# Kernel optimization log

Measured on AMD Instinct MI355X. Metric: run time of the kernel, lower is better.

Reference implementation:

```python
import jax, jax.numpy as jnp
import numpy as np

N_NODES = 50000
N_EDGES = 800000
F_DIM = 256
H_DIM = 256
O_DIM = 64


def spmm(edge_index, edge_weight, x):
    # sparse adj (COO) @ dense x: out[dst] += w * x[src]
    src = edge_index[0]
    dst = edge_index[1]
    msgs = edge_weight[:, None] * x[src]          # [E, D]
    return jax.ops.segment_sum(msgs, dst, num_segments=x.shape[0])


def setup_inputs() -> dict:
    key = jax.random.key(0)
    ks = jax.random.split(key, 10)
    stdv = 1.0 / np.sqrt(H_DIM)
    u = lambda k, shp: jax.random.uniform(k, shp, jnp.float32, -stdv, stdv)
    return {
        "input": jax.random.normal(ks[0], (N_NODES, F_DIM), jnp.float32),
        "edge_index": jax.random.randint(ks[1], (2, N_EDGES), 0, N_NODES, jnp.int32),
        "edge_weight": jax.random.uniform(ks[2], (N_EDGES,), jnp.float32),
        "mixture_weight": u(ks[3], (1,)),
        "hidden_weight": u(ks[4], (F_DIM, H_DIM)),
        "hidden_bias": u(ks[5], (H_DIM,)),
        "mean_weight": u(ks[6], (H_DIM, O_DIM)),
        "mean_bias": u(ks[7], (O_DIM,)),
        "log_std_weight": u(ks[8], (H_DIM, O_DIM)),
        "log_std_bias": u(ks[9], (O_DIM,)),
    }


def reference(input, edge_index, edge_weight, mixture_weight, hidden_weight,
              hidden_bias, mean_weight, mean_bias, log_std_weight, log_std_bias):
    # eval mode: dropout is identity
    # --- GCN branch ---
    support = input @ hidden_weight                       # [N, H]
    hidden_g = jax.nn.relu(spmm(edge_index, edge_weight, support) + hidden_bias)
    mean_gcn = spmm(edge_index, edge_weight, hidden_g @ mean_weight)      # [N, O]
    log_std_gcn = spmm(edge_index, edge_weight, hidden_g @ log_std_weight)
    # --- MLP branch ---
    hidden_m = jax.nn.relu(support + hidden_bias)
    mean_mlp = hidden_m @ mean_weight + mean_bias
    log_std_mlp = hidden_m @ log_std_weight + log_std_bias
    # --- mixture (note: z_mean uses raw weight, z_log_std uses sigmoid, as in source) ---
    mw = mixture_weight
    mr = jax.nn.sigmoid(mixture_weight)
    z_mean = mean_gcn * mw + mean_mlp * (1.0 - mw)
    z_log_std = log_std_gcn * mr + log_std_mlp * (1.0 - mr)
    return (z_mean, z_log_std)
```

## Files before the change

kernel.cpp:

```cpp
#include <hip/hip_runtime.h>
#include <math.h>

#define NN 50000
#define NE 800000
#define KD 256
#define OD 64
#define NCH ((NN + 255) / 256)
#define EPB 4096
#define NBLK ((NE + EPB - 1) / EPB)
#define NHT (NCH * NBLK)

#define QS 32.0f
#define IQS (1.0f / 32.0f)

using bf16x8 = __attribute__((ext_vector_type(8))) short;
using f32x4  = __attribute__((ext_vector_type(4))) float;

__device__ __forceinline__ unsigned short f2b(float x) {
    union { float f; unsigned u; } c; c.f = x;
    unsigned r = (c.u + 0x7FFF + ((c.u >> 16) & 1)) >> 16;
    return (unsigned short)r;
}
__device__ __forceinline__ float b2f(unsigned short b) {
    union { unsigned u; float f; } c; c.u = ((unsigned)b) << 16;
    return c.f;
}
__device__ __forceinline__ signed char quant8(float v) {
    int q = __float2int_rn(v * QS);
    q = q > 127 ? 127 : (q < -127 ? -127 : q);
    return (signed char)q;
}


__global__ __launch_bounds__(256) void k_hist(const int* __restrict__ dst,
                                              int* __restrict__ histT) {
    __shared__ int bins[NCH];
    int t = threadIdx.x, blk = blockIdx.x;
    if (t < NCH) bins[t] = 0;
    __syncthreads();
    int base = blk * EPB;
    #pragma unroll
    for (int i = 0; i < EPB / 256; ++i) {
        int e = base + i * 256 + t;
        if (e < NE) atomicAdd(&bins[dst[e] >> 8], 1);
    }
    __syncthreads();
    if (t < NCH) histT[t * NBLK + blk] = bins[t];
}

__global__ __launch_bounds__(256) void k_scanbins(int* __restrict__ histT,
                                                  int* __restrict__ binSum) {
    __shared__ int s[256];
    int bin = blockIdx.x, t = threadIdx.x;
    int v = (t < NBLK) ? histT[bin * NBLK + t] : 0;
    s[t] = v;
    __syncthreads();
    for (int o = 1; o < 256; o <<= 1) {
        int x = (t >= o) ? s[t - o] : 0;
        __syncthreads();
        s[t] += x;
        __syncthreads();
    }
    if (t < NBLK) histT[bin * NBLK + t] = s[t] - v;
    if (t == NBLK - 1) binSum[bin] = s[t];
}

__global__ void k_binscan(const int* __restrict__ binSum, int* __restrict__ binPrefix) {
    __shared__ int s[256];
    int t = threadIdx.x;
    int v = (t < NCH) ? binSum[t] : 0;
    s[t] = v;
    __syncthreads();
    for (int o = 1; o < 256; o <<= 1) {
        int x = (t >= o) ? s[t - o] : 0;
        __syncthreads();
        s[t] += x;
        __syncthreads();
    }
    if (t < NCH) binPrefix[t] = s[t] - v;
    if (t == NCH - 1) binPrefix[NCH] = s[t];
}

__global__ __launch_bounds__(256) void k_bucketw(const int* __restrict__ src,
                                                 const int* __restrict__ dst,
                                                 const float* __restrict__ w,
                                                 const int* __restrict__ histT,
                                                 const int* __restrict__ binPrefix,
                                                 int2* __restrict__ bkt) {
    __shared__ int cur[NCH];
    int t = threadIdx.x, blk = blockIdx.x;
    if (t < NCH) cur[t] = histT[t * NBLK + blk] + binPrefix[t];
    __syncthreads();
    int base = blk * EPB;
    #pragma unroll
    for (int i = 0; i < EPB / 256; ++i) {
        int e = base + i * 256 + t;
        if (e < NE) {
            int d = dst[e];
            int p = atomicAdd(&cur[d >> 8], 1);
            bkt[p] = make_int2((d << 16) | src[e], __float_as_int(w[e]));
        }
    }
}

__global__ __launch_bounds__(256) void k_deg2(const int2* __restrict__ bkt,
                                              const int* __restrict__ binPrefix,
                                              int* __restrict__ deg,
                                              int* __restrict__ chunkSum8) {
    __shared__ int cnt[256];
    __shared__ int s[256];
    int t = threadIdx.x, b = blockIdx.x;
    cnt[t] = 0;
    __syncthreads();
    int e0 = binPrefix[b], e1 = binPrefix[b + 1];
    for (int e = e0 + t; e < e1; e += 256)
        atomicAdd(&cnt[(((unsigned)bkt[e].x) >> 16) & 255], 1);
    __syncthreads();
    int node = b * 256 + t;
    int c = cnt[t];
    if (node < NN) deg[node] = c;
    s[t] = (node < NN) ? ((c + 7) & ~7) : 0;
    __syncthreads();
    for (int o = 128; o > 0; o >>= 1) {
        if (t < o) s[t] += s[t + o];
        __syncthreads();
    }
    if (t == 0) chunkSum8[b] = s[0];
}

__global__ void k_scan_chunks(const int* __restrict__ chunkSum8, int* __restrict__ chunkOff8) {
    __shared__ int s[256];
    int t = threadIdx.x;
    int v = (t < NCH) ? chunkSum8[t] : 0;
    s[t] = v;
    __syncthreads();
    for (int o = 1; o < 256; o <<= 1) {
        int x = (t >= o) ? s[t - o] : 0;
        __syncthreads();
        s[t] += x;
        __syncthreads();
    }
    if (t < NCH) chunkOff8[t] = s[t] - v;
    if (t == NCH - 1) chunkOff8[NCH] = s[t];
}

__global__ void k_scan_write8(const int* __restrict__ deg, const int* __restrict__ chunkOff8,
                              int* __restrict__ offsets8) {
    __shared__ int s[256];
    int b = blockIdx.x, t = threadIdx.x;
    int g = b * 256 + t;
    int v = (g < NN) ? ((deg[g] + 7) & ~7) : 0;
    s[t] = v;
    __syncthreads();
    for (int o = 1; o < 256; o <<= 1) {
        int x = (t >= o) ? s[t - o] : 0;
        __syncthreads();
        s[t] += x;
        __syncthreads();
    }
    int excl = s[t] - v + chunkOff8[b];
    if (g <= NN) offsets8[g] = excl;
}

__global__ __launch_bounds__(256) void k_place2(const int2* __restrict__ bkt,
                                                const int* __restrict__ binPrefix,
                                                const int* __restrict__ offsets8,
                                                int2* __restrict__ pedge) {
    __shared__ int ncur[256];
    int t = threadIdx.x, b = blockIdx.x;
    int node = b * 256 + t;
    ncur[t] = (node < NN) ? offsets8[node] : 0;
    __syncthreads();
    int e0 = binPrefix[b], e1 = binPrefix[b + 1];
    for (int e = e0 + t; e < e1; e += 256) {
        int2 v = bkt[e];
        int d = ((unsigned)v.x) >> 16;
        int p = atomicAdd(&ncur[d & 255], 1);
        pedge[p] = v;
    }
    __syncthreads();
    if (node < NN) {
        int p0 = ncur[t];
        int p1 = offsets8[node + 1];
        for (int p = p0; p < p1; ++p) pedge[p] = make_int2(0, 0);
    }
}


__global__ void k_convW(const float* __restrict__ hw, const float* __restrict__ mw_,
                        const float* __restrict__ lw,
                        unsigned short* __restrict__ Wht, unsigned short* __restrict__ Wmlt) {
    int idx = blockIdx.x * 256 + threadIdx.x;
    if (idx < 256 * 256) {
        int n = idx >> 8, k = idx & 255;
        Wht[(size_t)n * 256 + k] = f2b(hw[(size_t)k * 256 + n]);
    }
    if (idx < 128 * 256) {
        int n = idx >> 8, k = idx & 255;
        float v = (n < 64) ? mw_[(size_t)k * 64 + n] : lw[(size_t)k * 64 + (n - 64)];
        Wmlt[(size_t)n * 256 + k] = f2b(v);
    }
}


template <int AM, int EM>
__global__ __launch_bounds__(256) void k_gemm(const void* __restrict__ Ap,
                                              const unsigned short* __restrict__ Bt,
                                              const float* __restrict__ hbias,
                                              const float* __restrict__ mbias,
                                              const float* __restrict__ lbias,
                                              void* __restrict__ Outp,
                                              void* __restrict__ Outp2) {
    __shared__ unsigned short As[64 * 64];
    __shared__ unsigned short Bs[128 * 64];
    const int tid = threadIdx.x;
    const int row0 = blockIdx.x * 64;
    const int n0 = blockIdx.y * 128;
    const int lane = tid & 63;
    const int w = tid >> 6, wm = w >> 1, wn = w & 1;
    const int lr = lane & 15, lg = lane >> 4;
    const int rA = tid >> 2;
    const int qA = tid & 3;
    const int rB = tid >> 1;
    const int hB = tid & 1;

    f32x4 acc[2][4] = {};

    for (int k0 = 0; k0 < KD; k0 += 64) {
        {
            int gr = row0 + rA;
            unsigned short tmp[16];
            if (AM == 0) {
                const float* A = (const float*)Ap;
                if (gr < NN) {
                    #pragma unroll
                    for (int i = 0; i < 4; ++i) {
                        float4 v = *reinterpret_cast<const float4*>(
                            &A[(size_t)gr * KD + k0 + qA * 16 + i * 4]);
                        tmp[i * 4 + 0] = f2b(v.x); tmp[i * 4 + 1] = f2b(v.y);
                        tmp[i * 4 + 2] = f2b(v.z); tmp[i * 4 + 3] = f2b(v.w);
                    }
                } else {
                    #pragma unroll
                    for (int i = 0; i < 16; ++i) tmp[i] = 0;
                }
            } else {
                const unsigned short* A = (const unsigned short*)Ap;
                if (gr < NN) {
                    *reinterpret_cast<uint4*>(&tmp[0]) =
                        *reinterpret_cast<const uint4*>(&A[(size_t)gr * KD + k0 + qA * 16]);
                    *reinterpret_cast<uint4*>(&tmp[8]) =
                        *reinterpret_cast<const uint4*>(&A[(size_t)gr * KD + k0 + qA * 16 + 8]);
                    if (AM == 2) {
                        #pragma unroll
                        for (int i = 0; i < 4; ++i) {
                            float4 hb4 = *reinterpret_cast<const float4*>(&hbias[k0 + qA * 16 + i * 4]);
                            tmp[i * 4 + 0] = f2b(fmaxf(b2f(tmp[i * 4 + 0]) + hb4.x, 0.f));
                            tmp[i * 4 + 1] = f2b(fmaxf(b2f(tmp[i * 4 + 1]) + hb4.y, 0.f));
                            tmp[i * 4 + 2] = f2b(fmaxf(b2f(tmp[i * 4 + 2]) + hb4.z, 0.f));
                            tmp[i * 4 + 3] = f2b(fmaxf(b2f(tmp[i * 4 + 3]) + hb4.w, 0.f));
                        }
                    }
                } else {
                    #pragma unroll
                    for (int i = 0; i < 16; ++i) tmp[i] = 0;
                }
            }
            int s0 = (qA * 2) ^ (rA & 7);
            int s1 = (qA * 2 + 1) ^ (rA & 7);
            *reinterpret_cast<uint4*>(&As[rA * 64 + s0 * 8]) = *reinterpret_cast<const uint4*>(&tmp[0]);
            *reinterpret_cast<uint4*>(&As[rA * 64 + s1 * 8]) = *reinterpret_cast<const uint4*>(&tmp[8]);
        }
        {
            const unsigned short* B = Bt + (size_t)(n0 + rB) * KD + k0 + hB * 32;
            #pragma unroll
            for (int i = 0; i < 4; ++i) {
                uint4 u = *reinterpret_cast<const uint4*>(B + i * 8);
                int slot = (hB * 4 + i) ^ (rB & 7);
                *reinterpret_cast<uint4*>(&Bs[rB * 64 + slot * 8]) = u;
            }
        }
        __syncthreads();
        #pragma unroll
        for (int ks = 0; ks < 2; ++ks) {
            int slot = ks * 4 + lg;
            bf16x8 a[2], b[4];
            #pragma unroll
            for (int fm = 0; fm < 2; ++fm) {
                int ra = wm * 32 + fm * 16 + lr;
                a[fm] = *reinterpret_cast<const bf16x8*>(&As[ra * 64 + ((slot ^ (ra & 7))) * 8]);
            }
            #pragma unroll
            for (int fn = 0; fn < 4; ++fn) {
                int rb = wn * 64 + fn * 16 + lr;
                b[fn] = *reinterpret_cast<const bf16x8*>(&Bs[rb * 64 + ((slot ^ (rb & 7))) * 8]);
            }
            #pragma unroll
            for (int fm = 0; fm < 2; ++fm)
                #pragma unroll
                for (int fn = 0; fn < 4; ++fn)
                    acc[fm][fn] = __builtin_amdgcn_mfma_f32_16x16x32_bf16(a[fm], b[fn], acc[fm][fn], 0, 0, 0);
        }
        __syncthreads();
    }
    #pragma unroll
    for (int fm = 0; fm < 2; ++fm) {
        #pragma unroll
        for (int j = 0; j < 4; ++j) {
            int grow = row0 + wm * 32 + fm * 16 + lg * 4 + j;
            if (grow >= NN) continue;
            #pragma unroll
            for (int fn = 0; fn < 4; ++fn) {
                int gcol = n0 + wn * 64 + fn * 16 + lr;
                float v = acc[fm][fn][j];
                if (EM == 2) {
                    ((unsigned short*)Outp)[(size_t)grow * 256 + gcol] = f2b(v);
                    ((signed char*)Outp2)[(size_t)grow * 256 + gcol] = quant8(v);
                } else if (EM == 3) {
                    ((signed char*)Outp)[(size_t)grow * 128 + gcol] = quant8(v);
                } else {
                    float b = (gcol < 64) ? mbias[gcol] : lbias[gcol - 64];
                    ((unsigned short*)Outp)[(size_t)grow * 128 + gcol] = f2b(v + b);
                }
            }
        }
    }
}


__global__ __launch_bounds__(256) void k_spmm1(const int* __restrict__ off8,
                                               const int2* __restrict__ pedge,
                                               const unsigned* __restrict__ supq,
                                               const float* __restrict__ bias,
                                               unsigned short* __restrict__ hg) {
    int lane = threadIdx.x & 63;
    int d = blockIdx.x * 4 + (threadIdx.x >> 6);
    int e0 = off8[d], e1 = off8[d + 1];
    float a0 = 0.f, a1 = 0.f, a2 = 0.f, a3 = 0.f;
    for (int e = e0; e < e1; e += 8) {
        int2 E[8];
        unsigned U[8];
        #pragma unroll
        for (int i = 0; i < 8; ++i) E[i] = pedge[e + i];
        #pragma unroll
        for (int i = 0; i < 8; ++i) U[i] = supq[(size_t)(E[i].x & 0xffff) * 64 + lane];
        #pragma unroll
        for (int i = 0; i < 8; ++i) {
            float w = __int_as_float(E[i].y);
            unsigned u = U[i];
            a0 = fmaf(w, (float)((int)(signed char)(u)), a0);
            a1 = fmaf(w, (float)((int)(signed char)(u >> 8)), a1);
            a2 = fmaf(w, (float)((int)(signed char)(u >> 16)), a2);
            a3 = fmaf(w, (float)((int)(signed char)(u >> 24)), a3);
        }
    }
    float4 b = *reinterpret_cast<const float4*>(&bias[lane * 4]);
    ushort4 o;
    o.x = f2b(fmaxf(a0 * IQS + b.x, 0.f));
    o.y = f2b(fmaxf(a1 * IQS + b.y, 0.f));
    o.z = f2b(fmaxf(a2 * IQS + b.z, 0.f));
    o.w = f2b(fmaxf(a3 * IQS + b.w, 0.f));
    reinterpret_cast<ushort4*>(hg)[(size_t)d * 64 + lane] = o;
}


__global__ __launch_bounds__(256) void k_spmm2(const int* __restrict__ off8,
                                               const int2* __restrict__ pedge,
                                               const unsigned short* __restrict__ gq,
                                               const unsigned short* __restrict__ mlp,
                                               const float* __restrict__ mixw,
                                               float* __restrict__ out) {
    int lane = threadIdx.x & 63;
    int d = blockIdx.x * 4 + (threadIdx.x >> 6);
    int e0 = off8[d], e1 = off8[d + 1];
    float a0 = 0.f, a1 = 0.f;
    for (int e = e0; e < e1; e += 8) {
        int2 E[8];
        unsigned short U[8];
        #pragma unroll
        for (int i = 0; i < 8; ++i) E[i] = pedge[e + i];
        #pragma unroll
        for (int i = 0; i < 8; ++i) U[i] = gq[(size_t)(E[i].x & 0xffff) * 64 + lane];
        #pragma unroll
        for (int i = 0; i < 8; ++i) {
            float w = __int_as_float(E[i].y);
            a0 = fmaf(w, (float)((int)(signed char)(U[i] & 0xff)), a0);
            a1 = fmaf(w, (float)((int)(signed char)(U[i] >> 8)), a1);
        }
    }
    float g0 = a0 * IQS, g1 = a1 * IQS;
    ushort2 mu = reinterpret_cast<const ushort2*>(mlp)[(size_t)d * 64 + lane];
    float m0 = b2f(mu.x), m1 = b2f(mu.y);
    float mw = mixw[0];
    float mr = 1.f / (1.f + expf(-mw));
    int c = lane * 2;
    if (c < 64) {
        *reinterpret_cast<float2*>(out + (size_t)d * OD + c) =
            make_float2(g0 * mw + m0 * (1.f - mw), g1 * mw + m1 * (1.f - mw));
    } else {
        *reinterpret_cast<float2*>(out + (size_t)NN * OD + (size_t)d * OD + (c - 64)) =
            make_float2(g0 * mr + m0 * (1.f - mr), g1 * mr + m1 * (1.f - mr));
    }
}


extern "C" void kernel_launch(void* const* d_in, const int* in_sizes, int n_in,
                              void* d_out, int out_size, void* d_ws, size_t ws_size,
                              hipStream_t stream) {
    const float* input = (const float*)d_in[0];
    const int*   ei    = (const int*)d_in[1];
    const float* ew    = (const float*)d_in[2];
    const float* mixw  = (const float*)d_in[3];
    const float* hw    = (const float*)d_in[4];
    const float* hb    = (const float*)d_in[5];
    const float* mw_   = (const float*)d_in[6];
    const float* mb    = (const float*)d_in[7];
    const float* lw    = (const float*)d_in[8];
    const float* lb    = (const float*)d_in[9];
    float* out = (float*)d_out;

    const int* src = ei;
    const int* dst = ei + NE;

    char* ws = (char*)d_ws;
    size_t off = 0;
    auto alloc = [&](size_t bytes) -> void* {
        void* p = ws + off;
        off += (bytes + 255) & ~(size_t)255;
        return p;
    };
    int*   deg      = (int*)alloc((size_t)NN * 4);
    int*   offsets8 = (int*)alloc((size_t)(NN + 1) * 4);
    int*   chunkSum8= (int*)alloc((size_t)NCH * 4);
    int*   chunkOff8= (int*)alloc((size_t)(NCH + 1) * 4);
    int*   binSum   = (int*)alloc((size_t)NCH * 4);
    int*   binPrefix= (int*)alloc((size_t)(NCH + 1) * 4);
    int*   histT    = (int*)alloc((size_t)NHT * 4);
    int2*  bkt      = (int2*)alloc((size_t)NE * 8);
    int2*  pedge    = (int2*)alloc(((size_t)NE + 8 * NN) * 8);
    unsigned short* Wht  = (unsigned short*)alloc((size_t)256 * 256 * 2);
    unsigned short* Wmlt = (unsigned short*)alloc((size_t)128 * 256 * 2);
    unsigned short* support  = (unsigned short*)alloc((size_t)NN * KD * 2);
    signed char*    supq     = (signed char*)alloc((size_t)NN * KD);
    unsigned short* hidden_g = (unsigned short*)alloc((size_t)NN * KD * 2);
    signed char*    gcnq     = (signed char*)alloc((size_t)NN * 128);
    unsigned short* mlp      = (unsigned short*)alloc((size_t)NN * 128 * 2);

    k_hist<<<NBLK, 256, 0, stream>>>(dst, histT);
    k_scanbins<<<NCH, 256, 0, stream>>>(histT, binSum);
    k_binscan<<<1, 256, 0, stream>>>(binSum, binPrefix);
    k_bucketw<<<NBLK, 256, 0, stream>>>(src, dst, ew, histT, binPrefix, bkt);
    k_deg2<<<NCH, 256, 0, stream>>>(bkt, binPrefix, deg, chunkSum8);
    k_scan_chunks<<<1, 256, 0, stream>>>(chunkSum8, chunkOff8);
    k_scan_write8<<<NCH, 256, 0, stream>>>(deg, chunkOff8, offsets8);
    k_place2<<<NCH, 256, 0, stream>>>(bkt, binPrefix, offsets8, pedge);

    k_convW<<<256, 256, 0, stream>>>(hw, mw_, lw, Wht, Wmlt);

    int mblk = (NN + 63) / 64;
    k_gemm<0, 2><<<dim3(mblk, 2), 256, 0, stream>>>(input, Wht, hb, mb, lb, support, supq);
    k_spmm1<<<NN / 4, 256, 0, stream>>>(offsets8, pedge, (const unsigned*)supq, hb, hidden_g);
    k_gemm<1, 3><<<dim3(mblk, 1), 256, 0, stream>>>(hidden_g, Wmlt, hb, mb, lb, gcnq, nullptr);
    k_gemm<2, 4><<<dim3(mblk, 1), 256, 0, stream>>>(support, Wmlt, hb, mb, lb, mlp, nullptr);
    k_spmm2<<<NN / 4, 256, 0, stream>>>(offsets8, pedge, (const unsigned short*)gcnq, mlp, mixw, out);
}
```

Baseline: 166.0 us.

## Process two nodes per wave in SpMM, quantize hidden to int8, fuse scan into placement

Each SpMM wave now handles two destination nodes with interleaved edge loops, which exposes more independent gathers per wave. The first SpMM writes the hidden activations as unsigned int8 (scale 16) instead of bf16, and the second GEMM gains an int8 input mode that dequantizes on load. The per-chunk offset scan is folded into the placement kernel, which removes one launch and a round trip through offsets. The cost is lower precision in the hidden activations (they clip at 127/16) and more register pressure in the SpMM kernels.

```diff
diff --git a/kernel.cpp b/kernel.cpp
--- a/kernel.cpp
+++ b/kernel.cpp
@@ -12,6 +12,8 @@
 
 #define QS 32.0f
 #define IQS (1.0f / 32.0f)
+#define QS2 16.0f
+#define IQS2 (1.0f / 16.0f)
 
 using bf16x8 = __attribute__((ext_vector_type(8))) short;
 using f32x4  = __attribute__((ext_vector_type(4))) float;
@@ -29,6 +31,10 @@
     int q = __float2int_rn(v * QS);
     q = q > 127 ? 127 : (q < -127 ? -127 : q);
     return (signed char)q;
+}
+__device__ __forceinline__ unsigned quant16u(float v) {
+    int q = __float2int_rn(v * QS2);
+    return (unsigned)(q > 127 ? 127 : q);
 }
 
 
@@ -144,32 +150,29 @@
     if (t == NCH - 1) chunkOff8[NCH] = s[t];
 }
 
-__global__ void k_scan_write8(const int* __restrict__ deg, const int* __restrict__ chunkOff8,
-                              int* __restrict__ offsets8) {
+__global__ __launch_bounds__(256) void k_place2f(const int2* __restrict__ bkt,
+                                                 const int* __restrict__ binPrefix,
+                                                 const int* __restrict__ chunkOff8,
+                                                 const int* __restrict__ deg,
+                                                 int* __restrict__ offsets8,
+                                                 int2* __restrict__ pedge) {
     __shared__ int s[256];
-    int b = blockIdx.x, t = threadIdx.x;
-    int g = b * 256 + t;
-    int v = (g < NN) ? ((deg[g] + 7) & ~7) : 0;
-    s[t] = v;
-    __syncthreads();
-    for (int o = 1; o < 256; o <<= 1) {
-        int x = (t >= o) ? s[t - o] : 0;
-        __syncthreads();
-        s[t] += x;
-        __syncthreads();
-    }
-    int excl = s[t] - v + chunkOff8[b];
-    if (g <= NN) offsets8[g] = excl;
-}
-
-__global__ __launch_bounds__(256) void k_place2(const int2* __restrict__ bkt,
-                                                const int* __restrict__ binPrefix,
-                                                const int* __restrict__ offsets8,
-                                                int2* __restrict__ pedge) {
     __shared__ int ncur[256];
     int t = threadIdx.x, b = blockIdx.x;
     int node = b * 256 + t;
-    ncur[t] = (node < NN) ? offsets8[node] : 0;
+    int dv = (node < NN) ? deg[node] : 0;
+    int pv = (dv + 7) & ~7;
+    s[t] = pv;
+    __syncthreads();
+    for (int o = 1; o < 256; o <<= 1) {
+        int x = (t >= o) ? s[t - o] : 0;
+        __syncthreads();
+        s[t] += x;
+        __syncthreads();
+    }
+    int excl = s[t] - pv + chunkOff8[b];
+    if (node <= NN) offsets8[node] = excl;
+    ncur[t] = excl;
     __syncthreads();
     int e0 = binPrefix[b], e1 = binPrefix[b + 1];
     for (int e = e0 + t; e < e1; e += 256) {
@@ -181,7 +184,7 @@
     __syncthreads();
     if (node < NN) {
         int p0 = ncur[t];
-        int p1 = offsets8[node + 1];
+        int p1 = excl + pv;
         for (int p = p0; p < p1; ++p) pedge[p] = make_int2(0, 0);
     }
 }
@@ -244,23 +247,33 @@
                     #pragma unroll
                     for (int i = 0; i < 16; ++i) tmp[i] = 0;
                 }
-            } else {
+            } else if (AM == 2) {
                 const unsigned short* A = (const unsigned short*)Ap;
                 if (gr < NN) {
                     *reinterpret_cast<uint4*>(&tmp[0]) =
                         *reinterpret_cast<const uint4*>(&A[(size_t)gr * KD + k0 + qA * 16]);
                     *reinterpret_cast<uint4*>(&tmp[8]) =
                         *reinterpret_cast<const uint4*>(&A[(size_t)gr * KD + k0 + qA * 16 + 8]);
-                    if (AM == 2) {
-                        #pragma unroll
-                        for (int i = 0; i < 4; ++i) {
-                            float4 hb4 = *reinterpret_cast<const float4*>(&hbias[k0 + qA * 16 + i * 4]);
-                            tmp[i * 4 + 0] = f2b(fmaxf(b2f(tmp[i * 4 + 0]) + hb4.x, 0.f));
-                            tmp[i * 4 + 1] = f2b(fmaxf(b2f(tmp[i * 4 + 1]) + hb4.y, 0.f));
-                            tmp[i * 4 + 2] = f2b(fmaxf(b2f(tmp[i * 4 + 2]) + hb4.z, 0.f));
-                            tmp[i * 4 + 3] = f2b(fmaxf(b2f(tmp[i * 4 + 3]) + hb4.w, 0.f));
-                        }
+                    #pragma unroll
+                    for (int i = 0; i < 4; ++i) {
+                        float4 hb4 = *reinterpret_cast<const float4*>(&hbias[k0 + qA * 16 + i * 4]);
+                        tmp[i * 4 + 0] = f2b(fmaxf(b2f(tmp[i * 4 + 0]) + hb4.x, 0.f));
+                        tmp[i * 4 + 1] = f2b(fmaxf(b2f(tmp[i * 4 + 1]) + hb4.y, 0.f));
+                        tmp[i * 4 + 2] = f2b(fmaxf(b2f(tmp[i * 4 + 2]) + hb4.z, 0.f));
+                        tmp[i * 4 + 3] = f2b(fmaxf(b2f(tmp[i * 4 + 3]) + hb4.w, 0.f));
                     }
+                } else {
+                    #pragma unroll
+                    for (int i = 0; i < 16; ++i) tmp[i] = 0;
+                }
+            } else {
+                const signed char* A = (const signed char*)Ap;
+                if (gr < NN) {
+                    signed char q[16];
+                    *reinterpret_cast<uint4*>(q) =
+                        *reinterpret_cast<const uint4*>(&A[(size_t)gr * KD + k0 + qA * 16]);
+                    #pragma unroll
+                    for (int i = 0; i < 16; ++i) tmp[i] = f2b((float)q[i] * IQS2);
                 } else {
                     #pragma unroll
                     for (int i = 0; i < 16; ++i) tmp[i] = 0;
@@ -332,35 +345,79 @@
                                                const int2* __restrict__ pedge,
                                                const unsigned* __restrict__ supq,
                                                const float* __restrict__ bias,
-                                               unsigned short* __restrict__ hg) {
+                                               unsigned* __restrict__ hgq) {
     int lane = threadIdx.x & 63;
-    int d = blockIdx.x * 4 + (threadIdx.x >> 6);
-    int e0 = off8[d], e1 = off8[d + 1];
+    int wid = blockIdx.x * 4 + (threadIdx.x >> 6);
+    int d0 = wid * 2, d1 = d0 + 1;
+    int ea = off8[d0], eA = off8[d0 + 1], eB = off8[d0 + 2];
+    int eb = eA;
     float a0 = 0.f, a1 = 0.f, a2 = 0.f, a3 = 0.f;
-    for (int e = e0; e < e1; e += 8) {
-        int2 E[8];
-        unsigned U[8];
-        #pragma unroll
-        for (int i = 0; i < 8; ++i) E[i] = pedge[e + i];
+    float c0 = 0.f, c1 = 0.f, c2 = 0.f, c3 = 0.f;
+    for (; ea < eA && eb < eB; ea += 8, eb += 8) {
+        int2 Ea[8], Eb[8];
+        unsigned Ua[8], Ub[8];
+        #pragma unroll
+        for (int i = 0; i < 8; ++i) { Ea[i] = pedge[ea + i]; Eb[i] = pedge[eb + i]; }
+        #pragma unroll
+        for (int i = 0; i < 8; ++i) {
+            Ua[i] = supq[(size_t)(Ea[i].x & 0xffff) * 64 + lane];
+            Ub[i] = supq[(size_t)(Eb[i].x & 0xffff) * 64 + lane];
+        }
+        #pragma unroll
+        for (int i = 0; i < 8; ++i) {
+            float wa = __int_as_float(Ea[i].y), wb = __int_as_float(Eb[i].y);
+            unsigned ua = Ua[i], ub = Ub[i];
+            a0 = fmaf(wa, (float)((int)(signed char)(ua)), a0);
+            a1 = fmaf(wa, (float)((int)(signed char)(ua >> 8)), a1);
+            a2 = fmaf(wa, (float)((int)(signed char)(ua >> 16)), a2);
+            a3 = fmaf(wa, (float)((int)(signed char)(ua >> 24)), a3);
+            c0 = fmaf(wb, (float)((int)(signed char)(ub)), c0);
+            c1 = fmaf(wb, (float)((int)(signed char)(ub >> 8)), c1);
+            c2 = fmaf(wb, (float)((int)(signed char)(ub >> 16)), c2);
+            c3 = fmaf(wb, (float)((int)(signed char)(ub >> 24)), c3);
+        }
+    }
+    for (; ea < eA; ea += 8) {
+        int2 E[8]; unsigned U[8];
+        #pragma unroll
+        for (int i = 0; i < 8; ++i) E[i] = pedge[ea + i];
         #pragma unroll
         for (int i = 0; i < 8; ++i) U[i] = supq[(size_t)(E[i].x & 0xffff) * 64 + lane];
         #pragma unroll
         for (int i = 0; i < 8; ++i) {
-            float w = __int_as_float(E[i].y);
-            unsigned u = U[i];
+            float w = __int_as_float(E[i].y); unsigned u = U[i];
             a0 = fmaf(w, (float)((int)(signed char)(u)), a0);
             a1 = fmaf(w, (float)((int)(signed char)(u >> 8)), a1);
             a2 = fmaf(w, (float)((int)(signed char)(u >> 16)), a2);
             a3 = fmaf(w, (float)((int)(signed char)(u >> 24)), a3);
         }
     }
+    for (; eb < eB; eb += 8) {
+        int2 E[8]; unsigned U[8];
+        #pragma unroll
+        for (int i = 0; i < 8; ++i) E[i] = pedge[eb + i];
+        #pragma unroll
+        for (int i = 0; i < 8; ++i) U[i] = supq[(size_t)(E[i].x & 0xffff) * 64 + lane];
+        #pragma unroll
+        for (int i = 0; i < 8; ++i) {
+            float w = __int_as_float(E[i].y); unsigned u = U[i];
+            c0 = fmaf(w, (float)((int)(signed char)(u)), c0);
+            c1 = fmaf(w, (float)((int)(signed char)(u >> 8)), c1);
+            c2 = fmaf(w, (float)((int)(signed char)(u >> 16)), c2);
+            c3 = fmaf(w, (float)((int)(signed char)(u >> 24)), c3);
+        }
+    }
     float4 b = *reinterpret_cast<const float4*>(&bias[lane * 4]);
-    ushort4 o;
-    o.x = f2b(fmaxf(a0 * IQS + b.x, 0.f));
-    o.y = f2b(fmaxf(a1 * IQS + b.y, 0.f));
-    o.z = f2b(fmaxf(a2 * IQS + b.z, 0.f));
-    o.w = f2b(fmaxf(a3 * IQS + b.w, 0.f));
-    reinterpret_cast<ushort4*>(hg)[(size_t)d * 64 + lane] = o;
+    unsigned oa = quant16u(fmaxf(a0 * IQS + b.x, 0.f))
+                | (quant16u(fmaxf(a1 * IQS + b.y, 0.f)) << 8)
+                | (quant16u(fmaxf(a2 * IQS + b.z, 0.f)) << 16)
+                | (quant16u(fmaxf(a3 * IQS + b.w, 0.f)) << 24);
+    unsigned oc = quant16u(fmaxf(c0 * IQS + b.x, 0.f))
+                | (quant16u(fmaxf(c1 * IQS + b.y, 0.f)) << 8)
+                | (quant16u(fmaxf(c2 * IQS + b.z, 0.f)) << 16)
+                | (quant16u(fmaxf(c3 * IQS + b.w, 0.f)) << 24);
+    hgq[(size_t)d0 * 64 + lane] = oa;
+    hgq[(size_t)d1 * 64 + lane] = oc;
 }
 
 
@@ -371,14 +428,34 @@
                                                const float* __restrict__ mixw,
                                                float* __restrict__ out) {
     int lane = threadIdx.x & 63;
-    int d = blockIdx.x * 4 + (threadIdx.x >> 6);
-    int e0 = off8[d], e1 = off8[d + 1];
-    float a0 = 0.f, a1 = 0.f;
-    for (int e = e0; e < e1; e += 8) {
-        int2 E[8];
-        unsigned short U[8];
-        #pragma unroll
-        for (int i = 0; i < 8; ++i) E[i] = pedge[e + i];
+    int wid = blockIdx.x * 4 + (threadIdx.x >> 6);
+    int d0 = wid * 2, d1 = d0 + 1;
+    int ea = off8[d0], eA = off8[d0 + 1], eB = off8[d0 + 2];
+    int eb = eA;
+    float a0 = 0.f, a1 = 0.f, c0 = 0.f, c1 = 0.f;
+    for (; ea < eA && eb < eB; ea += 8, eb += 8) {
+        int2 Ea[8], Eb[8];
+        unsigned short Ua[8], Ub[8];
+        #pragma unroll
+        for (int i = 0; i < 8; ++i) { Ea[i] = pedge[ea + i]; Eb[i] = pedge[eb + i]; }
+        #pragma unroll
+        for (int i = 0; i < 8; ++i) {
+            Ua[i] = gq[(size_t)(Ea[i].x & 0xffff) * 64 + lane];
+            Ub[i] = gq[(size_t)(Eb[i].x & 0xffff) * 64 + lane];
+        }
+        #pragma unroll
+        for (int i = 0; i < 8; ++i) {
+            float wa = __int_as_float(Ea[i].y), wb = __int_as_float(Eb[i].y);
+            a0 = fmaf(wa, (float)((int)(signed char)(Ua[i] & 0xff)), a0);
+            a1 = fmaf(wa, (float)((int)(signed char)(Ua[i] >> 8)), a1);
+            c0 = fmaf(wb, (float)((int)(signed char)(Ub[i] & 0xff)), c0);
+            c1 = fmaf(wb, (float)((int)(signed char)(Ub[i] >> 8)), c1);
+        }
+    }
+    for (; ea < eA; ea += 8) {
+        int2 E[8]; unsigned short U[8];
+        #pragma unroll
+        for (int i = 0; i < 8; ++i) E[i] = pedge[ea + i];
         #pragma unroll
         for (int i = 0; i < 8; ++i) U[i] = gq[(size_t)(E[i].x & 0xffff) * 64 + lane];
         #pragma unroll
@@ -388,18 +465,37 @@
             a1 = fmaf(w, (float)((int)(signed char)(U[i] >> 8)), a1);
         }
     }
-    float g0 = a0 * IQS, g1 = a1 * IQS;
-    ushort2 mu = reinterpret_cast<const ushort2*>(mlp)[(size_t)d * 64 + lane];
-    float m0 = b2f(mu.x), m1 = b2f(mu.y);
+    for (; eb < eB; eb += 8) {
+        int2 E[8]; unsigned short U[8];
+        #pragma unroll
+        for (int i = 0; i < 8; ++i) E[i] = pedge[eb + i];
+        #pragma unroll
+        for (int i = 0; i < 8; ++i) U[i] = gq[(size_t)(E[i].x & 0xffff) * 64 + lane];
+        #pragma unroll
+        for (int i = 0; i < 8; ++i) {
+            float w = __int_as_float(E[i].y);
+            c0 = fmaf(w, (float)((int)(signed char)(U[i] & 0xff)), c0);
+            c1 = fmaf(w, (float)((int)(signed char)(U[i] >> 8)), c1);
+        }
+    }
     float mw = mixw[0];
     float mr = 1.f / (1.f + expf(-mw));
     int c = lane * 2;
+    ushort2 mu0 = reinterpret_cast<const ushort2*>(mlp)[(size_t)d0 * 64 + lane];
+    ushort2 mu1 = reinterpret_cast<const ushort2*>(mlp)[(size_t)d1 * 64 + lane];
+    float g00 = a0 * IQS, g01 = a1 * IQS;
+    float g10 = c0 * IQS, g11 = c1 * IQS;
     if (c < 64) {
-        *reinterpret_cast<float2*>(out + (size_t)d * OD + c) =
-            make_float2(g0 * mw + m0 * (1.f - mw), g1 * mw + m1 * (1.f - mw));
+        *reinterpret_cast<float2*>(out + (size_t)d0 * OD + c) =
+            make_float2(g00 * mw + b2f(mu0.x) * (1.f - mw), g01 * mw + b2f(mu0.y) * (1.f - mw));
+        *reinterpret_cast<float2*>(out + (size_t)d1 * OD + c) =
+            make_float2(g10 * mw + b2f(mu1.x) * (1.f - mw), g11 * mw + b2f(mu1.y) * (1.f - mw));
     } else {
-        *reinterpret_cast<float2*>(out + (size_t)NN * OD + (size_t)d * OD + (c - 64)) =
-            make_float2(g0 * mr + m0 * (1.f - mr), g1 * mr + m1 * (1.f - mr));
+        float* ol = out + (size_t)NN * OD;
+        *reinterpret_cast<float2*>(ol + (size_t)d0 * OD + (c - 64)) =
+            make_float2(g00 * mr + b2f(mu0.x) * (1.f - mr), g01 * mr + b2f(mu0.y) * (1.f - mr));
+        *reinterpret_cast<float2*>(ol + (size_t)d1 * OD + (c - 64)) =
+            make_float2(g10 * mr + b2f(mu1.x) * (1.f - mr), g11 * mr + b2f(mu1.y) * (1.f - mr));
     }
 }
 
@@ -430,7 +526,7 @@
         return p;
     };
     int*   deg      = (int*)alloc((size_t)NN * 4);
-    int*   offsets8 = (int*)alloc((size_t)(NN + 1) * 4);
+    int*   offsets8 = (int*)alloc((size_t)(NN + 2) * 4);
     int*   chunkSum8= (int*)alloc((size_t)NCH * 4);
     int*   chunkOff8= (int*)alloc((size_t)(NCH + 1) * 4);
     int*   binSum   = (int*)alloc((size_t)NCH * 4);
@@ -442,7 +538,7 @@
     unsigned short* Wmlt = (unsigned short*)alloc((size_t)128 * 256 * 2);
     unsigned short* support  = (unsigned short*)alloc((size_t)NN * KD * 2);
     signed char*    supq     = (signed char*)alloc((size_t)NN * KD);
-    unsigned short* hidden_g = (unsigned short*)alloc((size_t)NN * KD * 2);
+    signed char*    hgq      = (signed char*)alloc((size_t)NN * KD);
     signed char*    gcnq     = (signed char*)alloc((size_t)NN * 128);
     unsigned short* mlp      = (unsigned short*)alloc((size_t)NN * 128 * 2);
 
@@ -452,15 +548,14 @@
     k_bucketw<<<NBLK, 256, 0, stream>>>(src, dst, ew, histT, binPrefix, bkt);
     k_deg2<<<NCH, 256, 0, stream>>>(bkt, binPrefix, deg, chunkSum8);
     k_scan_chunks<<<1, 256, 0, stream>>>(chunkSum8, chunkOff8);
-    k_scan_write8<<<NCH, 256, 0, stream>>>(deg, chunkOff8, offsets8);
-    k_place2<<<NCH, 256, 0, stream>>>(bkt, binPrefix, offsets8, pedge);
+    k_place2f<<<NCH, 256, 0, stream>>>(bkt, binPrefix, chunkOff8, deg, offsets8, pedge);
 
     k_convW<<<256, 256, 0, stream>>>(hw, mw_, lw, Wht, Wmlt);
 
     int mblk = (NN + 63) / 64;
     k_gemm<0, 2><<<dim3(mblk, 2), 256, 0, stream>>>(input, Wht, hb, mb, lb, support, supq);
-    k_spmm1<<<NN / 4, 256, 0, stream>>>(offsets8, pedge, (const unsigned*)supq, hb, hidden_g);
-    k_gemm<1, 3><<<dim3(mblk, 1), 256, 0, stream>>>(hidden_g, Wmlt, hb, mb, lb, gcnq, nullptr);
+    k_spmm1<<<NN / 8, 256, 0, stream>>>(offsets8, pedge, (const unsigned*)supq, hb, (unsigned*)hgq);
+    k_gemm<4, 3><<<dim3(mblk, 1), 256, 0, stream>>>(hgq, Wmlt, hb, mb, lb, gcnq, nullptr);
     k_gemm<2, 4><<<dim3(mblk, 1), 256, 0, stream>>>(support, Wmlt, hb, mb, lb, mlp, nullptr);
-    k_spmm2<<<NN / 4, 256, 0, stream>>>(offsets8, pedge, (const unsigned short*)gcnq, mlp, mixw, out);
-}
+    k_spmm2<<<NN / 8, 256, 0, stream>>>(offsets8, pedge, (const unsigned short*)gcnq, mlp, mixw, out);
+}
```

After: 158.4 us. -4.5%, faster.
